# Performance work log

Hardware: AMD Instinct MI355X
Metric: run time of the kernel (lower is better)

The kernel has to match this reference:

```python
import jax, jax.numpy as jnp
import numpy as np


def _flip_roll(a):
    # torch.roll(torch.flip(a, [-3,-2,-1]), (1,1,1), [-3,-2,-1])
    return jnp.roll(jnp.flip(a, axis=(-3, -2, -1)), shift=(1, 1, 1), axis=(-3, -2, -1))


def dht_3d(x):
    dims = (2, 3, 4)
    r = jnp.fft.fftn(x, axes=dims).real - jnp.fft.fftn(jnp.flip(x, axis=-1), axes=dims).imag
    norm = jnp.sqrt(jnp.sum(r * r, axis=dims, keepdims=True))
    safe = jnp.where(norm == 0, 1.0, norm)
    return jnp.where(norm != 0, r / safe, jnp.zeros_like(r))


def compl_mul3d(x1, x2):
    x1n = _flip_roll(x1)
    x2n = _flip_roll(x2)
    return 0.5 * (
        jnp.einsum('bixyz,ioxyz->boxyz', x1, x2)
        - jnp.einsum('bixyz,ioxyz->boxyz', x1n, x2n)
        + jnp.einsum('bixyz,ioxyz->boxyz', x1, x2n)
        + jnp.einsum('bixyz,ioxyz->boxyz', x1n, x2)
    )


def idht_3d(X):
    n = X.shape[2] * X.shape[3] * X.shape[4]
    return dht_3d(X) / n


def setup_inputs() -> dict:
    key = jax.random.key(0)
    k1, k2 = jax.random.split(key)
    B, Cin, Cout = 4, 32, 32
    S = 64
    M = 8
    scale = 1.0 / (Cin * Cout)
    x = jax.random.normal(k1, (B, Cin, S, S, S), dtype=jnp.float32)
    weights1 = scale * jax.random.uniform(k2, (Cin, Cout, M, M, M), dtype=jnp.float32)
    return {"x": x, "weights1": weights1}


def reference(x, weights1):
    B = x.shape[0]
    Cout = weights1.shape[1]
    m1, m2, m3 = weights1.shape[2], weights1.shape[3], weights1.shape[4]
    s1, s2, s3 = x.shape[-3], x.shape[-2], x.shape[-1]
    x_ht = dht_3d(x)
    conv = compl_mul3d(x_ht[:, :, :m1, :m2, :m3], weights1)
    out_ht = jnp.zeros((B, Cout, s1, s2, s3), dtype=x.dtype)
    out_ht = out_ht.at[:, :, :m1, :m2, :m3].set(conv)
    return idht_3d(out_ht)
```

## Files before the change

kernel.cpp:

```cpp
#include <hip/hip_runtime.h>
#include <math.h>


constexpr int NT = 262144;
constexpr float TWOPI_64 = 0.09817477042468103f;


__global__ __launch_bounds__(256) void k_fwd1(const float* __restrict__ x,
                                              float* __restrict__ P,
                                              float* __restrict__ red1) {
  __shared__ float As[64 * 65];
  __shared__ float Bs[64 * 65];
  __shared__ float c64[64], s64[64];
  __shared__ float rsm[12];
  const int t = threadIdx.x;
  const int j = blockIdx.x;
  const int bc = blockIdx.y;
  const int n1a = j, n1b = (64 - j) & 63;
  const bool paired = (n1a != n1b);
  if (t < 64) { float ang = TWOPI_64 * t; c64[t] = cosf(ang); s64[t] = sinf(ang); }
  const float* xa = x + ((size_t)bc << 18) + (n1a << 12);
  const float* xb = x + ((size_t)bc << 18) + (n1b << 12);
  for (int q = 0; q < 16; ++q) {
    int l = t + (q << 8);
    int r = l >> 6, c = l & 63;
    As[r * 65 + c] = xa[l];
    Bs[r * 65 + c] = xb[l];
  }
  __syncthreads();
  {
    const int n2 = t & 63;
    const int k3a = t >> 6;
    const int k3b = k3a + 4;
    float ca = 1.f, sa = 0.f, cb = 1.f, sb = 0.f;
    const float dca = c64[k3a], dsa = s64[k3a];
    const float dcb = c64[k3b], dsb = s64[k3b];
    float reA0 = 0, imA0 = 0, reA1 = 0, imA1 = 0;
    float reB0 = 0, imB0 = 0, reB1 = 0, imB1 = 0;
    const float* Ar = &As[n2 * 65];
    const float* Br = &Bs[n2 * 65];
    for (int n3 = 0; n3 < 64; ++n3) {
      float va = Ar[n3], vb = Br[n3];
      reA0 += va * ca; imA0 -= va * sa;
      reB0 += vb * ca; imB0 -= vb * sa;
      reA1 += va * cb; imA1 -= va * sb;
      reB1 += vb * cb; imB1 -= vb * sb;
      float nca = ca * dca - sa * dsa; sa = sa * dca + ca * dsa; ca = nca;
      float ncb = cb * dcb - sb * dsb; sb = sb * dcb + cb * dsb; cb = ncb;
    }
    float2* Pp = (float2*)P;
    Pp[(((size_t)bc * 8 + k3a) * 64 + n1a) * 64 + n2] = make_float2(reA0, imA0);
    Pp[(((size_t)bc * 8 + k3b) * 64 + n1a) * 64 + n2] = make_float2(reA1, imA1);
    if (paired) {
      Pp[(((size_t)bc * 8 + k3a) * 64 + n1b) * 64 + n2] = make_float2(reB0, imB0);
      Pp[(((size_t)bc * 8 + k3b) * 64 + n1b) * 64 + n2] = make_float2(reB1, imB1);
    }
  }
  float ssp = 0.f, c1p = 0.f, c2p = 0.f;
  for (int q = 0; q < 16; ++q) {
    int l = t + (q << 8);
    int r = l >> 6, c = l & 63;
    float a = As[r * 65 + c];
    int m2 = (64 - r) & 63;
    int m3 = (64 - c) & 63;
    int m3b = (62 - c) & 63;
    float b1 = Bs[m2 * 65 + m3];
    float b2 = Bs[m2 * 65 + m3b];
    ssp += a * a;
    if (paired) { float bb = Bs[r * 65 + c]; ssp += bb * bb; }
    c1p += a * b1;
    c2p += a * b2;
  }
  if (paired) { c1p *= 2.f; c2p *= 2.f; }
  for (int off = 32; off; off >>= 1) {
    ssp += __shfl_down(ssp, off);
    c1p += __shfl_down(c1p, off);
    c2p += __shfl_down(c2p, off);
  }
  const int lane = t & 63, wid = t >> 6;
  if (lane == 0) { rsm[wid * 3] = ssp; rsm[wid * 3 + 1] = c1p; rsm[wid * 3 + 2] = c2p; }
  __syncthreads();
  if (t == 0) {
    atomicAdd(&red1[bc * 3 + 0], rsm[0] + rsm[3] + rsm[6] + rsm[9]);
    atomicAdd(&red1[bc * 3 + 1], rsm[1] + rsm[4] + rsm[7] + rsm[10]);
    atomicAdd(&red1[bc * 3 + 2], rsm[2] + rsm[5] + rsm[8] + rsm[11]);
  }
}

__global__ __launch_bounds__(256) void k_fwd2(const float* __restrict__ P,
                                              const float* __restrict__ red1,
                                              float* __restrict__ xh) {
  __shared__ float Pf[64 * 130];
  __shared__ float S2L[2048];
  __shared__ float U3L[256];
  __shared__ float c64[64], s64[64];
  const int t = threadIdx.x;
  const int k3 = blockIdx.x;
  const int bc = blockIdx.y;
  if (t < 64) { float ang = TWOPI_64 * t; c64[t] = cosf(ang); s64[t] = sinf(ang); }
  const float4* Pb4 = (const float4*)(P + ((size_t)(bc * 8 + k3) << 13));
  for (int q = 0; q < 8; ++q) {
    int l4 = t + (q << 8);
    float4 v = Pb4[l4];
    int fl = l4 << 2;
    int row = fl >> 7, col = fl & 127;
    float2* d = (float2*)&Pf[row * 130 + col];
    d[0] = make_float2(v.x, v.y);
    d[1] = make_float2(v.z, v.w);
  }
  __syncthreads();
  {
    const int n1 = t >> 2;
    const int f = (t >> 1) & 1;
    const int kh = t & 1;
    float are[4] = {0, 0, 0, 0}, aim[4] = {0, 0, 0, 0};
    float rc[4], rs_[4], dc[4], ds_[4];
#pragma unroll
    for (int q = 0; q < 4; ++q) {
      int k2 = 2 * q + kh;
      rc[q] = 1.f; rs_[q] = 0.f;
      dc[q] = c64[k2]; ds_[q] = s64[k2];
    }
    const float* col0 = &Pf[n1 * 130 + f];
    for (int n2 = 0; n2 < 64; ++n2) {
      float v = col0[2 * n2];
#pragma unroll
      for (int q = 0; q < 4; ++q) {
        are[q] += v * rc[q]; aim[q] -= v * rs_[q];
        float nc = rc[q] * dc[q] - rs_[q] * ds_[q];
        rs_[q] = rs_[q] * dc[q] + rc[q] * ds_[q];
        rc[q] = nc;
      }
    }
    float2* S2 = (float2*)S2L;
#pragma unroll
    for (int q = 0; q < 4; ++q) {
      int k2 = 2 * q + kh;
      S2[(n1 * 2 + f) * 8 + k2] = make_float2(are[q], aim[q]);
    }
  }
  __syncthreads();
  if (t < 128) {
    const int f = t >> 6, k1 = (t >> 3) & 7, k2 = t & 7;
    float rc = 1.f, rs2 = 0.f;
    const float dc = c64[k1], ds2 = s64[k1];
    float re = 0.f, im = 0.f;
    const float2* S2 = (const float2*)S2L;
    for (int n1 = 0; n1 < 64; ++n1) {
      float2 ab = S2[(n1 * 2 + f) * 8 + k2];
      re += ab.x * rc + ab.y * rs2;
      im += ab.y * rc - ab.x * rs2;
      float nc = rc * dc - rs2 * ds2;
      rs2 = rs2 * dc + rc * ds2;
      rc = nc;
    }
    ((float2*)U3L)[(f * 8 + k1) * 8 + k2] = make_float2(re, im);
  }
  __syncthreads();
  if (t < 64) {
    float ssv = red1[bc * 3], c1v = red1[bc * 3 + 1], c2v = red1[bc * 3 + 2];
    float nsq = 0.5f * (float)NT * (2.f * ssv + c1v - c2v);
    float inv1 = nsq > 0.f ? rsqrtf(nsq) : 0.f;
    const int k1 = t >> 3, k2 = t & 7;
    const float2* U3 = (const float2*)U3L;
    float2 U = U3[k1 * 8 + k2];
    float2 V = U3[64 + k1 * 8 + k2];
    float ct = c64[k3], st = s64[k3];
    float r = U.x - V.y - st * (U.x + V.y) - ct * (U.y - V.x);
    xh[bc * 512 + (k1 * 8 + k2) * 8 + k3] = r * inv1;
  }
}

__global__ __launch_bounds__(256) void k_mix(const float* __restrict__ xh,
                                             const float* __restrict__ w,
                                             float* __restrict__ convG) {
  __shared__ float xsh[16384];
  const int t = threadIdx.x;
  const int bc2 = blockIdx.x;
  const int b = bc2 >> 5, o = bc2 & 31;
  const float4* xb4 = (const float4*)(xh + ((size_t)b << 14));
  float4* xs4 = (float4*)xsh;
  for (int q = 0; q < 16; ++q) xs4[t + (q << 8)] = xb4[t + (q << 8)];
  __syncthreads();
  for (int q = 0; q < 2; ++q) {
    int k = t + (q << 8);
    int k1 = k >> 6, k2 = (k >> 3) & 7, k3 = k & 7;
    int nk = (((8 - k1) & 7) << 6) + (((8 - k2) & 7) << 3) + ((8 - k3) & 7);
    float acc = 0.f;
    for (int i = 0; i < 32; ++i) {
      float xa = xsh[(i << 9) + k];
      float xn = xsh[(i << 9) + nk];
      const float* wr = w + (((size_t)i * 32 + o) << 9);
      acc += (xa + xn) * wr[k] + (xa - xn) * wr[nk];
    }
    convG[((size_t)bc2 << 9) + k] = 0.5f * acc;
  }
}

__global__ __launch_bounds__(256) void k_expA(const float* __restrict__ convG,
                                              float* __restrict__ A1,
                                              float* __restrict__ inv2) {
  __shared__ float c64[64], s64[64];
  const int t = threadIdx.x;
  const int bc2 = blockIdx.x;
  if (t < 64) { float ang = TWOPI_64 * t; c64[t] = cosf(ang); s64[t] = sinf(ang); }
  const int col = t & 63;
  const int quarter = t >> 6;
  const float* cb = convG + ((size_t)bc2 << 9);
  float cv[8];
#pragma unroll
  for (int n1 = 0; n1 < 8; ++n1) cv[n1] = cb[(n1 << 6) + col];
  if (quarter == 0) {
    float p = 0.f;
#pragma unroll
    for (int n1 = 0; n1 < 8; ++n1) p += cv[n1] * cv[n1];
    for (int off = 32; off; off >>= 1) p += __shfl_down(p, off);
    if (t == 0) {
      float c000 = cv[0];
      float nsq = 0.5f * (float)NT * (2.f * p + c000 * c000);
      float nrm = sqrtf(nsq);
      inv2[bc2] = nrm > 0.f ? 1.f / (nrm * (float)NT) : 0.f;
    }
  }
  __syncthreads();
  float2* A1p = (float2*)(A1 + ((size_t)bc2 << 13));
  for (int it = 0; it < 16; ++it) {
    int k1 = quarter + (it << 2);
    float re = 0.f, im = 0.f;
#pragma unroll
    for (int n1 = 0; n1 < 8; ++n1) {
      int a = (k1 * n1) & 63;
      re += cv[n1] * c64[a];
      im -= cv[n1] * s64[a];
    }
    A1p[(k1 << 6) + col] = make_float2(re, im);
  }
}

__global__ __launch_bounds__(256) void k_expB(const float* __restrict__ A1,
                                              float* __restrict__ A2) {
  const int t = threadIdx.x;
  const int kh = blockIdx.x;
  const int bc2 = blockIdx.y;
  const int k2 = t & 63;
  const int wid = __builtin_amdgcn_readfirstlane(t >> 6);
  float ctw[8], stw[8];
#pragma unroll
  for (int n2 = 0; n2 < 8; ++n2) {
    float ang = TWOPI_64 * ((k2 * n2) & 63);
    ctw[n2] = cosf(ang); stw[n2] = sinf(ang);
  }
  const float* A1b = A1 + ((size_t)bc2 << 13);
  for (int it = 0; it < 8; ++it) {
    int k1 = kh * 32 + it * 4 + wid;
    const float* ar = A1b + (k1 << 7);
    float re[8] = {0, 0, 0, 0, 0, 0, 0, 0}, im[8] = {0, 0, 0, 0, 0, 0, 0, 0};
#pragma unroll
    for (int n2 = 0; n2 < 8; ++n2) {
      float tc = ctw[n2], ts = stw[n2];
#pragma unroll
      for (int n3 = 0; n3 < 8; ++n3) {
        float a = ar[(n2 * 8 + n3) * 2];
        float b = ar[(n2 * 8 + n3) * 2 + 1];
        re[n3] += a * tc + b * ts;
        im[n3] += b * tc - a * ts;
      }
    }
    float out16[16];
#pragma unroll
    for (int n3 = 0; n3 < 8; ++n3) { out16[n3 * 2] = re[n3]; out16[n3 * 2 + 1] = im[n3]; }
    float4* dst = (float4*)(A2 + ((((size_t)bc2 * 64 + k1) * 64 + k2) << 4));
    const float4* s4 = (const float4*)out16;
    dst[0] = s4[0]; dst[1] = s4[1]; dst[2] = s4[2]; dst[3] = s4[3];
  }
}

__global__ __launch_bounds__(256) void k_expC(const float* __restrict__ A2,
                                              const float* __restrict__ inv2,
                                              float* __restrict__ out) {
  const int t = threadIdx.x;
  const int k1 = blockIdx.x;
  const int bc2 = blockIdx.y;
  const int k3 = t & 63;
  const int wid = __builtin_amdgcn_readfirstlane(t >> 6);
  float C1r[8], C2r[8];
  {
    float cj[9], sj[9];
#pragma unroll
    for (int jj = 0; jj < 9; ++jj) {
      float ang = TWOPI_64 * ((k3 * jj) & 63);
      cj[jj] = cosf(ang); sj[jj] = sinf(ang);
    }
#pragma unroll
    for (int n3 = 0; n3 < 8; ++n3) {
      C1r[n3] = cj[n3] - sj[n3 + 1];
      C2r[n3] = sj[n3] - cj[n3 + 1];
    }
  }
  const float sc = inv2[bc2];
  const float* Ab = A2 + (((size_t)bc2 * 64 + k1) << 10);
  float* dst = out + ((size_t)bc2 << 18) + (k1 << 12);
  for (int it = 0; it < 16; ++it) {
    int k2 = wid * 16 + it;
    const float* ar = Ab + (k2 << 4);
    float acc = 0.f;
#pragma unroll
    for (int n3 = 0; n3 < 8; ++n3)
      acc += ar[n3 * 2] * C1r[n3] + ar[n3 * 2 + 1] * C2r[n3];
    dst[(k2 << 6) + k3] = acc * sc;
  }
}

extern "C" void kernel_launch(void* const* d_in, const int* in_sizes, int n_in,
                              void* d_out, int out_size, void* d_ws, size_t ws_size,
                              hipStream_t stream) {
  const float* x = (const float*)d_in[0];
  const float* w = (const float*)d_in[1];
  float* out = (float*)d_out;
  float* ws = (float*)d_ws;
  float* P    = ws + 0;
  float* red1 = ws + 8388608;
  float* xh   = ws + 8388992;
  float* conv = ws + 8454528;
  float* inv2 = ws + 8520064;
  float* A1   = ws + 8520192;
  float* A2   = ws + 0;

  hipMemsetAsync(red1, 0, 384 * sizeof(float), stream);
  k_fwd1<<<dim3(33, 128), 256, 0, stream>>>(x, P, red1);
  k_fwd2<<<dim3(8, 128), 256, 0, stream>>>(P, red1, xh);
  k_mix<<<dim3(128), 256, 0, stream>>>(xh, w, conv);
  k_expA<<<dim3(128), 256, 0, stream>>>(conv, A1, inv2);
  k_expB<<<dim3(2, 128), 256, 0, stream>>>(A1, A2);
  k_expC<<<dim3(64, 128), 256, 0, stream>>>(A2, inv2, out);
}
```

Before: 335.2 us.

## Fuse DHT pipeline stages into four kernels and reduce intermediate traffic

Folds the n2 DFT into k_fwd1 through a shared-memory stage, so it writes a smaller S buffer instead of the full P intermediate. It also vectorises x loads with float4 and computes the sum of squares during the load. Per-block partial reductions now go to a buffer instead of atomics, which removes the memset. k_mix is fused with k_expA, and k_expB with k_expC, so the convG and A2 round trips through global memory disappear. In exchange k_fwd2s runs on only 128 blocks with a longer serial loop, and k_expBC recomputes its B2 stage in every block.

```diff
diff --git a/kernel.cpp b/kernel.cpp
--- a/kernel.cpp
+++ b/kernel.cpp
@@ -7,69 +7,73 @@
 
 
 __global__ __launch_bounds__(256) void k_fwd1(const float* __restrict__ x,
-                                              float* __restrict__ P,
-                                              float* __restrict__ red1) {
-  __shared__ float As[64 * 65];
-  __shared__ float Bs[64 * 65];
-  __shared__ float c64[64], s64[64];
+                                              float* __restrict__ S,
+                                              float* __restrict__ red1p) {
+  __shared__ float As[64 * 68];
+  __shared__ float Bs[64 * 68];
+  __shared__ float PL[32 * 65];
+  __shared__ float c64v[64], s64v[64];
   __shared__ float rsm[12];
   const int t = threadIdx.x;
   const int j = blockIdx.x;
   const int bc = blockIdx.y;
   const int n1a = j, n1b = (64 - j) & 63;
   const bool paired = (n1a != n1b);
-  if (t < 64) { float ang = TWOPI_64 * t; c64[t] = cosf(ang); s64[t] = sinf(ang); }
-  const float* xa = x + ((size_t)bc << 18) + (n1a << 12);
-  const float* xb = x + ((size_t)bc << 18) + (n1b << 12);
+  if (t < 64) { float ang = TWOPI_64 * t; c64v[t] = cosf(ang); s64v[t] = sinf(ang); }
+  const float4* xa4 = (const float4*)(x + ((size_t)bc << 18) + (n1a << 12));
+  const float4* xb4 = (const float4*)(x + ((size_t)bc << 18) + (n1b << 12));
+  float ssp = 0.f;
+  for (int q = 0; q < 4; ++q) {
+    int l4 = t + (q << 8);
+    int fl = l4 << 2;
+    int r = fl >> 6, c = fl & 63;
+    float4 va = xa4[l4], vb = xb4[l4];
+    *(float4*)&As[r * 68 + c] = va;
+    *(float4*)&Bs[r * 68 + c] = vb;
+    ssp += va.x * va.x + va.y * va.y + va.z * va.z + va.w * va.w;
+    if (paired) ssp += vb.x * vb.x + vb.y * vb.y + vb.z * vb.z + vb.w * vb.w;
+  }
+  __syncthreads();
+  const int n2 = t & 63;
+  const int k3a = t >> 6, k3b = k3a + 4;
+  {
+    float ca = 1.f, sa = 0.f, cb = 1.f, sb = 0.f;
+    const float dca = c64v[k3a], dsa = s64v[k3a];
+    const float dcb = c64v[k3b], dsb = s64v[k3b];
+    float reA0 = 0, imA0 = 0, reA1 = 0, imA1 = 0;
+    float reB0 = 0, imB0 = 0, reB1 = 0, imB1 = 0;
+    const float4* Ar = (const float4*)&As[n2 * 68];
+    const float4* Br = (const float4*)&Bs[n2 * 68];
+    for (int m = 0; m < 16; ++m) {
+      float4 va = Ar[m], vb = Br[m];
+      float av[4] = {va.x, va.y, va.z, va.w};
+      float bv[4] = {vb.x, vb.y, vb.z, vb.w};
+#pragma unroll
+      for (int e = 0; e < 4; ++e) {
+        float a = av[e], b = bv[e];
+        reA0 += a * ca; imA0 -= a * sa;
+        reB0 += b * ca; imB0 -= b * sa;
+        reA1 += a * cb; imA1 -= a * sb;
+        reB1 += b * cb; imB1 -= b * sb;
+        float nca = ca * dca - sa * dsa; sa = sa * dca + ca * dsa; ca = nca;
+        float ncb = cb * dcb - sb * dsb; sb = sb * dcb + cb * dsb; cb = ncb;
+      }
+    }
+    PL[(k3a) * 65 + n2] = reA0;      PL[(8 + k3a) * 65 + n2] = imA0;
+    PL[(16 + k3a) * 65 + n2] = reB0; PL[(24 + k3a) * 65 + n2] = imB0;
+    PL[(k3b) * 65 + n2] = reA1;      PL[(8 + k3b) * 65 + n2] = imA1;
+    PL[(16 + k3b) * 65 + n2] = reB1; PL[(24 + k3b) * 65 + n2] = imB1;
+  }
+  float c1p = 0.f, c2p = 0.f;
   for (int q = 0; q < 16; ++q) {
     int l = t + (q << 8);
     int r = l >> 6, c = l & 63;
-    As[r * 65 + c] = xa[l];
-    Bs[r * 65 + c] = xb[l];
-  }
-  __syncthreads();
-  {
-    const int n2 = t & 63;
-    const int k3a = t >> 6;
-    const int k3b = k3a + 4;
-    float ca = 1.f, sa = 0.f, cb = 1.f, sb = 0.f;
-    const float dca = c64[k3a], dsa = s64[k3a];
-    const float dcb = c64[k3b], dsb = s64[k3b];
-    float reA0 = 0, imA0 = 0, reA1 = 0, imA1 = 0;
-    float reB0 = 0, imB0 = 0, reB1 = 0, imB1 = 0;
-    const float* Ar = &As[n2 * 65];
-    const float* Br = &Bs[n2 * 65];
-    for (int n3 = 0; n3 < 64; ++n3) {
-      float va = Ar[n3], vb = Br[n3];
-      reA0 += va * ca; imA0 -= va * sa;
-      reB0 += vb * ca; imB0 -= vb * sa;
-      reA1 += va * cb; imA1 -= va * sb;
-      reB1 += vb * cb; imB1 -= vb * sb;
-      float nca = ca * dca - sa * dsa; sa = sa * dca + ca * dsa; ca = nca;
-      float ncb = cb * dcb - sb * dsb; sb = sb * dcb + cb * dsb; cb = ncb;
-    }
-    float2* Pp = (float2*)P;
-    Pp[(((size_t)bc * 8 + k3a) * 64 + n1a) * 64 + n2] = make_float2(reA0, imA0);
-    Pp[(((size_t)bc * 8 + k3b) * 64 + n1a) * 64 + n2] = make_float2(reA1, imA1);
-    if (paired) {
-      Pp[(((size_t)bc * 8 + k3a) * 64 + n1b) * 64 + n2] = make_float2(reB0, imB0);
-      Pp[(((size_t)bc * 8 + k3b) * 64 + n1b) * 64 + n2] = make_float2(reB1, imB1);
-    }
-  }
-  float ssp = 0.f, c1p = 0.f, c2p = 0.f;
-  for (int q = 0; q < 16; ++q) {
-    int l = t + (q << 8);
-    int r = l >> 6, c = l & 63;
-    float a = As[r * 65 + c];
+    float a = As[r * 68 + c];
     int m2 = (64 - r) & 63;
     int m3 = (64 - c) & 63;
     int m3b = (62 - c) & 63;
-    float b1 = Bs[m2 * 65 + m3];
-    float b2 = Bs[m2 * 65 + m3b];
-    ssp += a * a;
-    if (paired) { float bb = Bs[r * 65 + c]; ssp += bb * bb; }
-    c1p += a * b1;
-    c2p += a * b2;
+    c1p += a * Bs[m2 * 68 + m3];
+    c2p += a * Bs[m2 * 68 + m3b];
   }
   if (paired) { c1p *= 2.f; c2p *= 2.f; }
   for (int off = 32; off; off >>= 1) {
@@ -81,99 +85,94 @@
   if (lane == 0) { rsm[wid * 3] = ssp; rsm[wid * 3 + 1] = c1p; rsm[wid * 3 + 2] = c2p; }
   __syncthreads();
   if (t == 0) {
-    atomicAdd(&red1[bc * 3 + 0], rsm[0] + rsm[3] + rsm[6] + rsm[9]);
-    atomicAdd(&red1[bc * 3 + 1], rsm[1] + rsm[4] + rsm[7] + rsm[10]);
-    atomicAdd(&red1[bc * 3 + 2], rsm[2] + rsm[5] + rsm[8] + rsm[11]);
-  }
-}
-
-__global__ __launch_bounds__(256) void k_fwd2(const float* __restrict__ P,
-                                              const float* __restrict__ red1,
-                                              float* __restrict__ xh) {
-  __shared__ float Pf[64 * 130];
-  __shared__ float S2L[2048];
-  __shared__ float U3L[256];
-  __shared__ float c64[64], s64[64];
+    red1p[((size_t)bc * 33 + j) * 3 + 0] = rsm[0] + rsm[3] + rsm[6] + rsm[9];
+    red1p[((size_t)bc * 33 + j) * 3 + 1] = rsm[1] + rsm[4] + rsm[7] + rsm[10];
+    red1p[((size_t)bc * 33 + j) * 3 + 2] = rsm[2] + rsm[5] + rsm[8] + rsm[11];
+  }
+  {
+    const int k2 = t & 7;
+    const int rr = t >> 3;
+    const int row = rr >> 4, f = (rr >> 3) & 1, k3 = rr & 7;
+    float rc = 1.f, rs = 0.f;
+    const float dc = c64v[k2], ds = s64v[k2];
+    float re = 0.f, im = 0.f;
+    const float* pr = &PL[rr * 65];
+    for (int n2i = 0; n2i < 64; ++n2i) {
+      float v = pr[n2i];
+      re += v * rc; im -= v * rs;
+      float nc = rc * dc - rs * ds; rs = rs * dc + rc * ds; rc = nc;
+    }
+    const int n1row = row ? n1b : n1a;
+    ((float2*)S)[(((size_t)bc * 64 + n1row) * 2 + f) * 64 + k2 * 8 + k3] =
+        make_float2(re, im);
+  }
+}
+
+__global__ __launch_bounds__(256) void k_fwd2s(const float* __restrict__ S,
+                                               const float* __restrict__ red1p,
+                                               float* __restrict__ xh) {
+  __shared__ float2 U3L[1024];
+  __shared__ float c64v[64], s64v[64];
+  __shared__ float rbuf[99];
   const int t = threadIdx.x;
-  const int k3 = blockIdx.x;
-  const int bc = blockIdx.y;
-  if (t < 64) { float ang = TWOPI_64 * t; c64[t] = cosf(ang); s64[t] = sinf(ang); }
-  const float4* Pb4 = (const float4*)(P + ((size_t)(bc * 8 + k3) << 13));
-  for (int q = 0; q < 8; ++q) {
-    int l4 = t + (q << 8);
-    float4 v = Pb4[l4];
-    int fl = l4 << 2;
-    int row = fl >> 7, col = fl & 127;
-    float2* d = (float2*)&Pf[row * 130 + col];
-    d[0] = make_float2(v.x, v.y);
-    d[1] = make_float2(v.z, v.w);
-  }
-  __syncthreads();
-  {
-    const int n1 = t >> 2;
-    const int f = (t >> 1) & 1;
-    const int kh = t & 1;
-    float are[4] = {0, 0, 0, 0}, aim[4] = {0, 0, 0, 0};
-    float rc[4], rs_[4], dc[4], ds_[4];
-#pragma unroll
-    for (int q = 0; q < 4; ++q) {
-      int k2 = 2 * q + kh;
-      rc[q] = 1.f; rs_[q] = 0.f;
-      dc[q] = c64[k2]; ds_[q] = s64[k2];
-    }
-    const float* col0 = &Pf[n1 * 130 + f];
-    for (int n2 = 0; n2 < 64; ++n2) {
-      float v = col0[2 * n2];
-#pragma unroll
-      for (int q = 0; q < 4; ++q) {
-        are[q] += v * rc[q]; aim[q] -= v * rs_[q];
-        float nc = rc[q] * dc[q] - rs_[q] * ds_[q];
-        rs_[q] = rs_[q] * dc[q] + rc[q] * ds_[q];
-        rc[q] = nc;
+  const int bc = blockIdx.x;
+  if (t < 64) { float ang = TWOPI_64 * t; c64v[t] = cosf(ang); s64v[t] = sinf(ang); }
+  if (t < 99) rbuf[t] = red1p[(size_t)bc * 99 + t];
+  __syncthreads();
+  {
+    const int rr2 = t & 127;
+    const int k1g = t >> 7;
+    const float2* Sb = (const float2*)(S + ((size_t)bc << 14));
+    float rc[4], rs[4], dc[4], ds[4], re[4], im[4];
+#pragma unroll
+    for (int m = 0; m < 4; ++m) {
+      int k1 = k1g * 4 + m;
+      rc[m] = 1.f; rs[m] = 0.f; dc[m] = c64v[k1]; ds[m] = s64v[k1];
+      re[m] = 0.f; im[m] = 0.f;
+    }
+#pragma unroll 4
+    for (int n1 = 0; n1 < 64; ++n1) {
+      float2 ab = Sb[(n1 << 7) + rr2];
+#pragma unroll
+      for (int m = 0; m < 4; ++m) {
+        re[m] += ab.x * rc[m] + ab.y * rs[m];
+        im[m] += ab.y * rc[m] - ab.x * rs[m];
+        float nc = rc[m] * dc[m] - rs[m] * ds[m];
+        rs[m] = rs[m] * dc[m] + rc[m] * ds[m];
+        rc[m] = nc;
       }
     }
-    float2* S2 = (float2*)S2L;
-#pragma unroll
-    for (int q = 0; q < 4; ++q) {
-      int k2 = 2 * q + kh;
-      S2[(n1 * 2 + f) * 8 + k2] = make_float2(are[q], aim[q]);
-    }
-  }
-  __syncthreads();
-  if (t < 128) {
-    const int f = t >> 6, k1 = (t >> 3) & 7, k2 = t & 7;
-    float rc = 1.f, rs2 = 0.f;
-    const float dc = c64[k1], ds2 = s64[k1];
-    float re = 0.f, im = 0.f;
-    const float2* S2 = (const float2*)S2L;
-    for (int n1 = 0; n1 < 64; ++n1) {
-      float2 ab = S2[(n1 * 2 + f) * 8 + k2];
-      re += ab.x * rc + ab.y * rs2;
-      im += ab.y * rc - ab.x * rs2;
-      float nc = rc * dc - rs2 * ds2;
-      rs2 = rs2 * dc + rc * ds2;
-      rc = nc;
-    }
-    ((float2*)U3L)[(f * 8 + k1) * 8 + k2] = make_float2(re, im);
-  }
-  __syncthreads();
-  if (t < 64) {
-    float ssv = red1[bc * 3], c1v = red1[bc * 3 + 1], c2v = red1[bc * 3 + 2];
-    float nsq = 0.5f * (float)NT * (2.f * ssv + c1v - c2v);
-    float inv1 = nsq > 0.f ? rsqrtf(nsq) : 0.f;
-    const int k1 = t >> 3, k2 = t & 7;
-    const float2* U3 = (const float2*)U3L;
-    float2 U = U3[k1 * 8 + k2];
-    float2 V = U3[64 + k1 * 8 + k2];
-    float ct = c64[k3], st = s64[k3];
+    const int f = rr2 >> 6, k2 = (rr2 >> 3) & 7, k3 = rr2 & 7;
+#pragma unroll
+    for (int m = 0; m < 4; ++m) {
+      int k1 = k1g * 4 + m;
+      U3L[f * 512 + k1 * 64 + k2 * 8 + k3] = make_float2(re[m], im[m]);
+    }
+  }
+  __syncthreads();
+  float ss = 0.f, c1 = 0.f, c2 = 0.f;
+  for (int jj = 0; jj < 33; ++jj) {
+    ss += rbuf[jj * 3];
+    c1 += rbuf[jj * 3 + 1];
+    c2 += rbuf[jj * 3 + 2];
+  }
+  float nsq = 0.5f * (float)NT * (2.f * ss + c1 - c2);
+  float inv1 = nsq > 0.f ? rsqrtf(nsq) : 0.f;
+  for (int q = 0; q < 2; ++q) {
+    int kk = t + (q << 8);
+    int k1 = kk >> 6, k2 = (kk >> 3) & 7, k3 = kk & 7;
+    float2 U = U3L[k1 * 64 + k2 * 8 + k3];
+    float2 V = U3L[512 + k1 * 64 + k2 * 8 + k3];
+    float ct = c64v[k3], st = s64v[k3];
     float r = U.x - V.y - st * (U.x + V.y) - ct * (U.y - V.x);
-    xh[bc * 512 + (k1 * 8 + k2) * 8 + k3] = r * inv1;
-  }
-}
-
-__global__ __launch_bounds__(256) void k_mix(const float* __restrict__ xh,
-                                             const float* __restrict__ w,
-                                             float* __restrict__ convG) {
+    xh[(size_t)bc * 512 + kk] = r * inv1;
+  }
+}
+
+__global__ __launch_bounds__(256) void k_mixA(const float* __restrict__ xh,
+                                              const float* __restrict__ w,
+                                              float* __restrict__ A1,
+                                              float* __restrict__ inv2) {
   __shared__ float xsh[16384];
   const int t = threadIdx.x;
   const int bc2 = blockIdx.x;
@@ -182,34 +181,35 @@
   float4* xs4 = (float4*)xsh;
   for (int q = 0; q < 16; ++q) xs4[t + (q << 8)] = xb4[t + (q << 8)];
   __syncthreads();
-  for (int q = 0; q < 2; ++q) {
-    int k = t + (q << 8);
-    int k1 = k >> 6, k2 = (k >> 3) & 7, k3 = k & 7;
-    int nk = (((8 - k1) & 7) << 6) + (((8 - k2) & 7) << 3) + ((8 - k3) & 7);
-    float acc = 0.f;
+  float acc0 = 0.f, acc1 = 0.f;
+  {
+    int k0 = t, kq1 = t + 256;
+    int k1 = k0 >> 6, k2 = (k0 >> 3) & 7, k3 = k0 & 7;
+    int nk0 = (((8 - k1) & 7) << 6) + (((8 - k2) & 7) << 3) + ((8 - k3) & 7);
+    int l1 = kq1 >> 6, l2 = (kq1 >> 3) & 7, l3 = kq1 & 7;
+    int nk1 = (((8 - l1) & 7) << 6) + (((8 - l2) & 7) << 3) + ((8 - l3) & 7);
     for (int i = 0; i < 32; ++i) {
-      float xa = xsh[(i << 9) + k];
-      float xn = xsh[(i << 9) + nk];
       const float* wr = w + (((size_t)i * 32 + o) << 9);
-      acc += (xa + xn) * wr[k] + (xa - xn) * wr[nk];
-    }
-    convG[((size_t)bc2 << 9) + k] = 0.5f * acc;
-  }
-}
-
-__global__ __launch_bounds__(256) void k_expA(const float* __restrict__ convG,
-                                              float* __restrict__ A1,
-                                              float* __restrict__ inv2) {
-  __shared__ float c64[64], s64[64];
-  const int t = threadIdx.x;
-  const int bc2 = blockIdx.x;
-  if (t < 64) { float ang = TWOPI_64 * t; c64[t] = cosf(ang); s64[t] = sinf(ang); }
+      float xa0 = xsh[(i << 9) + k0],  xn0 = xsh[(i << 9) + nk0];
+      float xa1 = xsh[(i << 9) + kq1], xn1 = xsh[(i << 9) + nk1];
+      acc0 += (xa0 + xn0) * wr[k0]  + (xa0 - xn0) * wr[nk0];
+      acc1 += (xa1 + xn1) * wr[kq1] + (xa1 - xn1) * wr[nk1];
+    }
+  }
+  __syncthreads();
+  xsh[t] = 0.5f * acc0;
+  xsh[t + 256] = 0.5f * acc1;
+  if (t < 64) {
+    float ang = TWOPI_64 * t;
+    xsh[512 + t] = cosf(ang);
+    xsh[576 + t] = sinf(ang);
+  }
+  __syncthreads();
   const int col = t & 63;
   const int quarter = t >> 6;
-  const float* cb = convG + ((size_t)bc2 << 9);
   float cv[8];
 #pragma unroll
-  for (int n1 = 0; n1 < 8; ++n1) cv[n1] = cb[(n1 << 6) + col];
+  for (int n1 = 0; n1 < 8; ++n1) cv[n1] = xsh[(n1 << 6) + col];
   if (quarter == 0) {
     float p = 0.f;
 #pragma unroll
@@ -222,7 +222,6 @@
       inv2[bc2] = nrm > 0.f ? 1.f / (nrm * (float)NT) : 0.f;
     }
   }
-  __syncthreads();
   float2* A1p = (float2*)(A1 + ((size_t)bc2 << 13));
   for (int it = 0; it < 16; ++it) {
     int k1 = quarter + (it << 2);
@@ -230,84 +229,67 @@
 #pragma unroll
     for (int n1 = 0; n1 < 8; ++n1) {
       int a = (k1 * n1) & 63;
-      re += cv[n1] * c64[a];
-      im -= cv[n1] * s64[a];
+      re += cv[n1] * xsh[512 + a];
+      im -= cv[n1] * xsh[576 + a];
     }
     A1p[(k1 << 6) + col] = make_float2(re, im);
   }
 }
 
-__global__ __launch_bounds__(256) void k_expB(const float* __restrict__ A1,
-                                              float* __restrict__ A2) {
-  const int t = threadIdx.x;
-  const int kh = blockIdx.x;
-  const int bc2 = blockIdx.y;
-  const int k2 = t & 63;
-  const int wid = __builtin_amdgcn_readfirstlane(t >> 6);
-  float ctw[8], stw[8];
-#pragma unroll
-  for (int n2 = 0; n2 < 8; ++n2) {
-    float ang = TWOPI_64 * ((k2 * n2) & 63);
-    ctw[n2] = cosf(ang); stw[n2] = sinf(ang);
-  }
-  const float* A1b = A1 + ((size_t)bc2 << 13);
-  for (int it = 0; it < 8; ++it) {
-    int k1 = kh * 32 + it * 4 + wid;
-    const float* ar = A1b + (k1 << 7);
-    float re[8] = {0, 0, 0, 0, 0, 0, 0, 0}, im[8] = {0, 0, 0, 0, 0, 0, 0, 0};
-#pragma unroll
-    for (int n2 = 0; n2 < 8; ++n2) {
-      float tc = ctw[n2], ts = stw[n2];
-#pragma unroll
-      for (int n3 = 0; n3 < 8; ++n3) {
-        float a = ar[(n2 * 8 + n3) * 2];
-        float b = ar[(n2 * 8 + n3) * 2 + 1];
-        re[n3] += a * tc + b * ts;
-        im[n3] += b * tc - a * ts;
-      }
-    }
-    float out16[16];
-#pragma unroll
-    for (int n3 = 0; n3 < 8; ++n3) { out16[n3 * 2] = re[n3]; out16[n3 * 2 + 1] = im[n3]; }
-    float4* dst = (float4*)(A2 + ((((size_t)bc2 * 64 + k1) * 64 + k2) << 4));
-    const float4* s4 = (const float4*)out16;
-    dst[0] = s4[0]; dst[1] = s4[1]; dst[2] = s4[2]; dst[3] = s4[3];
-  }
-}
-
-__global__ __launch_bounds__(256) void k_expC(const float* __restrict__ A2,
-                                              const float* __restrict__ inv2,
-                                              float* __restrict__ out) {
+__global__ __launch_bounds__(256) void k_expBC(const float* __restrict__ A1,
+                                               const float* __restrict__ inv2,
+                                               float* __restrict__ out) {
+  __shared__ float arow[128];
+  __shared__ float B2[64 * 17];
+  __shared__ float c64v[64], s64v[64];
   const int t = threadIdx.x;
   const int k1 = blockIdx.x;
   const int bc2 = blockIdx.y;
-  const int k3 = t & 63;
-  const int wid = __builtin_amdgcn_readfirstlane(t >> 6);
-  float C1r[8], C2r[8];
-  {
-    float cj[9], sj[9];
-#pragma unroll
-    for (int jj = 0; jj < 9; ++jj) {
-      float ang = TWOPI_64 * ((k3 * jj) & 63);
-      cj[jj] = cosf(ang); sj[jj] = sinf(ang);
-    }
+  if (t < 64) { float ang = TWOPI_64 * t; c64v[t] = cosf(ang); s64v[t] = sinf(ang); }
+  if (t < 128) arow[t] = A1[((size_t)bc2 << 13) + (k1 << 7) + t];
+  __syncthreads();
+  {
+    const int k2 = t & 63;
+    const int g = t >> 6;
+    const int f = g & 1;
+    const int n3h = (g >> 1) << 2;
+    float acc[4] = {0, 0, 0, 0};
+    for (int n2i = 0; n2i < 8; ++n2i) {
+      int a_ = (k2 * n2i) & 63;
+      float tc = c64v[a_], ts = s64v[a_];
+#pragma unroll
+      for (int e = 0; e < 4; ++e) {
+        int n3 = n3h + e;
+        float a = arow[((n2i << 3) + n3) << 1];
+        float b = arow[(((n2i << 3) + n3) << 1) + 1];
+        acc[e] += (f == 0) ? (a * tc + b * ts) : (b * tc - a * ts);
+      }
+    }
+#pragma unroll
+    for (int e = 0; e < 4; ++e) B2[k2 * 17 + (f << 3) + n3h + e] = acc[e];
+  }
+  __syncthreads();
+  {
+    const int k3 = t & 63;
+    const int wid = t >> 6;
+    float C1r[8], C2r[8];
 #pragma unroll
     for (int n3 = 0; n3 < 8; ++n3) {
-      C1r[n3] = cj[n3] - sj[n3 + 1];
-      C2r[n3] = sj[n3] - cj[n3 + 1];
-    }
-  }
-  const float sc = inv2[bc2];
-  const float* Ab = A2 + (((size_t)bc2 * 64 + k1) << 10);
-  float* dst = out + ((size_t)bc2 << 18) + (k1 << 12);
-  for (int it = 0; it < 16; ++it) {
-    int k2 = wid * 16 + it;
-    const float* ar = Ab + (k2 << 4);
-    float acc = 0.f;
-#pragma unroll
-    for (int n3 = 0; n3 < 8; ++n3)
-      acc += ar[n3 * 2] * C1r[n3] + ar[n3 * 2 + 1] * C2r[n3];
-    dst[(k2 << 6) + k3] = acc * sc;
+      int a0 = (k3 * n3) & 63;
+      int a1 = (k3 * (n3 + 1)) & 63;
+      C1r[n3] = c64v[a0] - s64v[a1];
+      C2r[n3] = s64v[a0] - c64v[a1];
+    }
+    const float sc = inv2[bc2];
+    float* dst = out + ((size_t)bc2 << 18) + (k1 << 12);
+    for (int it = 0; it < 16; ++it) {
+      int k2 = (wid << 4) + it;
+      const float* br = &B2[k2 * 17];
+      float acc = 0.f;
+#pragma unroll
+      for (int n3 = 0; n3 < 8; ++n3) acc += br[n3] * C1r[n3] + br[8 + n3] * C2r[n3];
+      dst[(k2 << 6) + k3] = acc * sc;
+    }
   }
 }
 
@@ -318,19 +300,14 @@
   const float* w = (const float*)d_in[1];
   float* out = (float*)d_out;
   float* ws = (float*)d_ws;
-  float* P    = ws + 0;
-  float* red1 = ws + 8388608;
-  float* xh   = ws + 8388992;
-  float* conv = ws + 8454528;
-  float* inv2 = ws + 8520064;
-  float* A1   = ws + 8520192;
-  float* A2   = ws + 0;
-
-  hipMemsetAsync(red1, 0, 384 * sizeof(float), stream);
-  k_fwd1<<<dim3(33, 128), 256, 0, stream>>>(x, P, red1);
-  k_fwd2<<<dim3(8, 128), 256, 0, stream>>>(P, red1, xh);
-  k_mix<<<dim3(128), 256, 0, stream>>>(xh, w, conv);
-  k_expA<<<dim3(128), 256, 0, stream>>>(conv, A1, inv2);
-  k_expB<<<dim3(2, 128), 256, 0, stream>>>(A1, A2);
-  k_expC<<<dim3(64, 128), 256, 0, stream>>>(A2, inv2, out);
-}
+  float* S     = ws;
+  float* red1p = ws + 2097152;
+  float* xh    = ws + 2109824;
+  float* inv2  = ws + 2175360;
+  float* A1    = ws + 2175488;
+
+  k_fwd1 <<<dim3(33, 128), 256, 0, stream>>>(x, S, red1p);
+  k_fwd2s<<<dim3(128),     256, 0, stream>>>(S, red1p, xh);
+  k_mixA <<<dim3(128),     256, 0, stream>>>(xh, w, A1, inv2);
+  k_expBC<<<dim3(64, 128), 256, 0, stream>>>(A1, inv2, out);
+}
```

Measured after the change: 280.8 us. 16.2% less time.
